# Performance work log

Hardware: AMD Instinct MI355X
Metric: run time of the kernel (lower is better)

Reference implementation:

```python
import jax, jax.numpy as jnp
import numpy as np

K = 16  # neighbors

def _pdist2(a, b):
    # squared euclidean distances (B,N,M); same argsort order as torch.cdist
    return (jnp.sum(a * a, -1)[:, :, None] + jnp.sum(b * b, -1)[:, None, :]
            - 2.0 * jnp.einsum('bnd,bmd->bnm', a, b))

def _knn(xyz, k):
    d2 = jax.lax.stop_gradient(_pdist2(xyz, xyz))
    return jax.lax.top_k(-d2, k)[1]  # (B,N,k) smallest distances

_gather_f = jax.vmap(lambda f, i: f[:, i])  # feat (C,N), idx (...,) -> (C,...)
_gather_x = jax.vmap(lambda x, i: x[i])     # xyz (N,D), idx (...,) -> (...,D)

def _bn_act(x, g, b):
    # eval-mode BatchNorm (running_mean=0, running_var=1) folded to affine, + LeakyReLU(0.1)
    shp = (1, -1) + (1,) * (x.ndim - 2)
    return jax.nn.leaky_relu(x * g.reshape(shp) + b.reshape(shp), 0.1)

def _lfa(xyz, feat, idx, Wm, gm, bm, Ws, Wp, gp, bp):
    # xyz (B,N,3), feat (B,C,N), idx (B,N,K)
    neigh_feat = _gather_f(feat, idx)          # (B,C,N,K)
    neigh_xyz = _gather_x(xyz, idx)            # (B,N,K,3)
    center = xyz[:, :, None, :]
    diff = center - neigh_xyz
    dist = jnp.linalg.norm(diff, axis=-1, keepdims=True)
    rel = jnp.concatenate([diff, dist, jnp.broadcast_to(center, neigh_xyz.shape), neigh_xyz], axis=-1)
    rel = jnp.transpose(rel, (0, 3, 1, 2))     # (B,10,N,K)
    x = jnp.concatenate([neigh_feat, rel], axis=1)          # (B,C+10,N,K)
    x = _bn_act(jnp.einsum('oc,bcnk->bonk', Wm, x), gm, bm)  # (B,O,N,K)
    a = jax.nn.softmax(jnp.einsum('oc,bcnk->bonk', Ws, x), axis=3)
    x = jnp.sum(x * a, axis=3)                               # attentive pool over K -> (B,O,N)
    return _bn_act(jnp.einsum('oc,bcn->bon', Wp, x), gp, bp)

def _interp(src_xyz, src_feat, tgt_xyz):
    nn_idx = jnp.argmin(jax.lax.stop_gradient(_pdist2(tgt_xyz, src_xyz)), axis=-1)  # (B,N)
    return _gather_f(src_feat, nn_idx)  # (B,C,N)


def setup_inputs() -> dict:
    key = jax.random.key(0)
    ks = jax.random.split(key, 24)
    B, N, CIN, NC = 2, 8192, 6, 13
    M1, M2 = N // 2, N // 4
    w = lambda i, shp: jax.random.normal(ks[i], shp, jnp.float32) * 0.05
    ones = lambda c: jnp.ones((c,), jnp.float32)
    zeros = lambda c: jnp.zeros((c,), jnp.float32)
    inp = {
        'xyz': jax.random.uniform(ks[0], (B, N, 3), jnp.float32),
        'feat': jax.random.normal(ks[1], (B, N, CIN), jnp.float32),
        'sel1': jax.random.randint(ks[2], (B, M1), 0, N),
        'sel2': jax.random.randint(ks[3], (B, M2), 0, M1),
        'Wpre': w(4, (64, CIN)), 'gpre': ones(64), 'bpre': zeros(64),
        'W1m': w(5, (64, 74)), 'g1m': ones(64), 'b1m': zeros(64),
        'W1s': w(6, (64, 64)), 'W1p': w(7, (64, 64)), 'g1p': ones(64), 'b1p': zeros(64),
        'W2m': w(8, (128, 74)), 'g2m': ones(128), 'b2m': zeros(128),
        'W2s': w(9, (128, 128)), 'W2p': w(10, (128, 128)), 'g2p': ones(128), 'b2p': zeros(128),
        'W3m': w(11, (256, 138)), 'g3m': ones(256), 'b3m': zeros(256),
        'W3s': w(12, (256, 256)), 'W3p': w(13, (256, 256)), 'g3p': ones(256), 'b3p': zeros(256),
        'Wu2': w(14, (128, 384)), 'gu2': ones(128), 'bu2': zeros(128),
        'Wu1': w(15, (64, 192)), 'gu1': ones(64), 'bu1': zeros(64),
        'Wh1': w(16, (64, 64)), 'bh1': zeros(64),
        'Wh2': w(17, (NC, 64)), 'bh2': zeros(NC),
    }
    return inp


def reference(xyz, feat, sel1, sel2, Wpre, gpre, bpre,
              W1m, g1m, b1m, W1s, W1p, g1p, b1p,
              W2m, g2m, b2m, W2s, W2p, g2p, b2p,
              W3m, g3m, b3m, W3s, W3p, g3p, b3p,
              Wu2, gu2, bu2, Wu1, gu1, bu1,
              Wh1, bh1, Wh2, bh2):
    ft = jnp.transpose(feat, (0, 2, 1))                       # (B,Cin,N)
    x0 = _bn_act(jnp.einsum('oc,bcn->bon', Wpre, ft), gpre, bpre)
    n0 = _knn(xyz, K)
    x1 = _lfa(xyz, x0, n0, W1m, g1m, b1m, W1s, W1p, g1p, b1p)  # (B,64,N)
    xyz1 = _gather_x(xyz, sel1); f1 = _gather_f(x1, sel1)      # random downsample 0.5
    n1 = _knn(xyz1, K)
    x2 = _lfa(xyz1, f1, n1, W2m, g2m, b2m, W2s, W2p, g2p, b2p)  # (B,128,M1)
    xyz2 = _gather_x(xyz1, sel2); f2 = _gather_f(x2, sel2)
    n2 = _knn(xyz2, K)
    x3 = _lfa(xyz2, f2, n2, W3m, g3m, b3m, W3s, W3p, g3p, b3p)  # (B,256,M2)
    up2 = _interp(xyz2, x3, xyz1)
    d2 = _bn_act(jnp.einsum('oc,bcn->bon', Wu2, jnp.concatenate([up2, x2], 1)), gu2, bu2)
    up1 = _interp(xyz1, d2, xyz)
    d1 = _bn_act(jnp.einsum('oc,bcn->bon', Wu1, jnp.concatenate([up1, x1], 1)), gu1, bu1)
    h = jax.nn.leaky_relu(jnp.einsum('oc,bcn->bon', Wh1, d1) + bh1[None, :, None], 0.1)
    logits = jnp.einsum('oc,bcn->bon', Wh2, h) + bh2[None, :, None]
    return jnp.transpose(logits, (0, 2, 1))                    # (B,N,num_classes)
```

## Files before the change

kernel.cpp:

```cpp
#include <hip/hip_runtime.h>
#include <hip/hip_bf16.h>

#pragma clang fp contract(off)

typedef unsigned long long ull;

__device__ __forceinline__ float lrelu(float v) { return v >= 0.0f ? v : 0.1f * v; }

__device__ __forceinline__ float sumsq3(float x, float y, float z) {
    return ((x * x) + (y * y)) + (z * z);
}

__device__ __forceinline__ float dot3fma(float ax, float ay, float az,
                                         float bx, float by, float bz) {
    float d = ax * bx;
    d = __builtin_fmaf(ay, by, d);
    d = __builtin_fmaf(az, bz, d);
    return d;
}

__device__ __forceinline__ float distf(float qn, float sn, float dot) {
    float s = qn + sn;
    return __builtin_fmaf(-2.0f, dot, s);
}

__device__ __forceinline__ ull packkey(float d, int i) {
    unsigned u = __float_as_uint(d);
    u = (u & 0x80000000u) ? ~u : (u | 0x80000000u);
    return ((ull)u << 32) | (unsigned)i;
}

__device__ __forceinline__ ull shfl_xor_u64(ull v, int mask) {
    int lo = __shfl_xor((int)(v & 0xffffffffull), mask);
    int hi = __shfl_xor((int)(v >> 32), mask);
    return ((ull)(unsigned)hi << 32) | (unsigned)lo;
}

__device__ __forceinline__ void cswap64(ull& x, ull& y) {
    bool sw = y < x;
    ull lo = sw ? y : x;
    ull hi = sw ? x : y;
    x = lo; y = hi;
}

__device__ __forceinline__ ull min64(ull a, ull b) { return a < b ? a : b; }

__global__ void k_pre(const float* __restrict__ feat, const float* __restrict__ W,
                      const float* __restrict__ g, const float* __restrict__ bb,
                      float* __restrict__ x0) {
    int p = blockIdx.x * blockDim.x + threadIdx.x;
    if (p >= 2 * 8192) return;
    const float* f = feat + (size_t)p * 6;
    float fv[6];
#pragma unroll
    for (int c = 0; c < 6; ++c) fv[c] = f[c];
    float* out = x0 + (size_t)p * 64;
    for (int o = 0; o < 64; ++o) {
        float s = 0.0f;
#pragma unroll
        for (int c = 0; c < 6; ++c) s = __builtin_fmaf(W[o * 6 + c], fv[c], s);
        float v = s * g[o];
        v = v + bb[o];
        out[o] = lrelu(v);
    }
}

__global__ void k_wt_all(const float* __restrict__ s0, const float* __restrict__ s1,
                         const float* __restrict__ s2, const float* __restrict__ s3,
                         const float* __restrict__ s4, const float* __restrict__ s5,
                         const float* __restrict__ s6, const float* __restrict__ s7,
                         const float* __restrict__ s8,
                         float* __restrict__ d0, float* __restrict__ d1,
                         float* __restrict__ d2, float* __restrict__ d3,
                         float* __restrict__ d4, float* __restrict__ d5,
                         float* __restrict__ d6, float* __restrict__ d7,
                         float* __restrict__ d8) {
    const int Ms[9] = {64, 64, 64, 128, 128, 128, 256, 256, 256};
    const int Ks[9] = {74, 64, 64, 74, 128, 128, 138, 256, 256};
    const float* S[9] = {s0, s1, s2, s3, s4, s5, s6, s7, s8};
    float* D[9] = {d0, d1, d2, d3, d4, d5, d6, d7, d8};
    int seg = blockIdx.y;
    int M = Ms[seg], K = Ks[seg];
    int i = blockIdx.x * 256 + threadIdx.x;
    if (i >= M * K) return;
    int o = i / K, c = i - o * K;
    D[seg][c * M + o] = S[seg][i];
}

template <int LPQ, int TS>
__launch_bounds__(256)
__global__ void k_knn_reg(const float* __restrict__ xyz, int* __restrict__ out_idx, int Npts) {
    constexpr int QPB = 256 / LPQ;
    __shared__ float4 sp[TS];
    int b = blockIdx.y;
    int tid = threadIdx.x;
    int qi = tid / LPQ;
    int l = tid % LPQ;
    int q = blockIdx.x * QPB + qi;
    const float* X = xyz + (size_t)b * Npts * 3;
    float qx = X[q * 3], qy = X[q * 3 + 1], qz = X[q * 3 + 2];
    float qn = sumsq3(qx, qy, qz);

    ull key[16];
#pragma unroll
    for (int u = 0; u < 16; ++u) key[u] = ~0ull;
    ull p0 = ~0ull, p1 = ~0ull, p2 = ~0ull, p3 = ~0ull;
    int cnt = 0;
    float tau_d = INFINITY;

    auto merge = [&]() {
        cswap64(p0, p2); cswap64(p1, p3); cswap64(p0, p1);
        cswap64(p2, p3); cswap64(p1, p2);
        key[12] = min64(key[12], p3);
        key[13] = min64(key[13], p2);
        key[14] = min64(key[14], p1);
        key[15] = min64(key[15], p0);
#pragma unroll
        for (int dstep = 8; dstep >= 1; dstep >>= 1) {
#pragma unroll
            for (int i = 0; i < 16; ++i) {
                if (!(i & dstep)) cswap64(key[i], key[i + dstep]);
            }
        }
        p0 = p1 = p2 = p3 = ~0ull;
        cnt = 0;
        ull t = key[15];
#pragma unroll
        for (int mask = 1; mask < LPQ; mask <<= 1) t = min64(t, shfl_xor_u64(t, mask));
        unsigned hu = (unsigned)(t >> 32);
        unsigned fb = (hu & 0x80000000u) ? (hu & 0x7fffffffu) : ~hu;
        tau_d = (hu == 0xffffffffu) ? INFINITY : __uint_as_float(fb);
    };

    for (int t0 = 0; t0 < Npts; t0 += TS) {
        __syncthreads();
        for (int j = tid; j < TS; j += 256) {
            int i = t0 + j;
            float px = X[i * 3], py = X[i * 3 + 1], pz = X[i * 3 + 2];
            sp[j] = make_float4(px, py, pz, sumsq3(px, py, pz));
        }
        __syncthreads();
        for (int j = l; j < TS; j += LPQ) {
            float4 p = sp[j];
            float d = distf(qn, p.w, dot3fma(qx, qy, qz, p.x, p.y, p.z));
            if (d <= tau_d) {
                p3 = p2; p2 = p1; p1 = p0;
                p0 = packkey(d, t0 + j);
                ++cnt;
            }
            if (__any(cnt >= 4)) merge();
        }
    }
    if (__any(cnt > 0)) merge();

    for (int mask = 1; mask < LPQ; mask <<= 1) {
        ull ok[16];
#pragma unroll
        for (int i = 0; i < 16; ++i) ok[i] = shfl_xor_u64(key[15 - i], mask);
#pragma unroll
        for (int i = 0; i < 16; ++i) key[i] = min64(ok[i], key[i]);
#pragma unroll
        for (int dstep = 8; dstep >= 1; dstep >>= 1) {
#pragma unroll
            for (int i = 0; i < 16; ++i) {
                if (!(i & dstep)) cswap64(key[i], key[i + dstep]);
            }
        }
    }

    if (l == 0) {
        int* o = out_idx + ((size_t)b * Npts + q) * 16;
#pragma unroll
        for (int u = 0; u < 16; ++u) o[u] = (int)(unsigned)(key[u] & 0xffffffffull);
    }
}

template <int C>
__global__ void k_gather(const float* __restrict__ src_xyz, const float* __restrict__ src_feat,
                         const int* __restrict__ sel, float* __restrict__ dst_xyz,
                         float* __restrict__ dst_feat, int M, int Nsrc) {
    int b = blockIdx.y, m = blockIdx.x;
    int s = sel[(size_t)b * M + m];
    const float* fx = src_xyz + ((size_t)b * Nsrc + s) * 3;
    const float* ff = src_feat + ((size_t)b * Nsrc + s) * C;
    float* dx = dst_xyz + ((size_t)b * M + m) * 3;
    float* df = dst_feat + ((size_t)b * M + m) * C;
    if (threadIdx.x < 3) dx[threadIdx.x] = fx[threadIdx.x];
    for (int c = threadIdx.x; c < C; c += blockDim.x) df[c] = ff[c];
}

template <int CIN, int COUT, int NCOL, int THREADS>
__launch_bounds__(THREADS)
__global__ void k_lfa(const float* __restrict__ xyz, const float* __restrict__ feat,
                      const int* __restrict__ kn,
                      const float* __restrict__ WmT, const float* __restrict__ gm, const float* __restrict__ bm,
                      const float* __restrict__ WsT,
                      const float* __restrict__ WpT, const float* __restrict__ gp, const float* __restrict__ bp,
                      float* __restrict__ outf, int Npts) {
    constexpr int CR = CIN + 10;
    constexpr int PPB = NCOL / 16;
    constexpr int BANDS = THREADS / 16;
    constexpr int RT = COUT / BANDS;
    constexpr int CT = NCOL / 16;
    constexpr int TPG = 16 / CT;
    constexpr int BUFR = (CR > COUT) ? CR : COUT;
    static_assert(RT % 4 == 0 && CT % 4 == 0, "geom");
    __shared__ __align__(16) float buf[BUFR * NCOL];
    int b = blockIdx.y, tid = threadIdx.x;
    int n0 = blockIdx.x * PPB;
    const float* X = xyz + (size_t)b * Npts * 3;

    {
        constexpr int TPC = THREADS / NCOL;
        int jl = tid % NCOL;
        int cp = tid / NCOL;
        int n = n0 + (jl >> 4);
        int k = jl & 15;
        int nbr = kn[((size_t)b * Npts + n) * 16 + k];
        const float* fr = feat + ((size_t)b * Npts + nbr) * CIN;
        for (int c = cp; c < CIN; c += TPC) buf[c * NCOL + jl] = fr[c];
        if (cp == 0) {
            float cx = X[n * 3], cy = X[n * 3 + 1], cz = X[n * 3 + 2];
            float nx = X[nbr * 3], ny = X[nbr * 3 + 1], nz = X[nbr * 3 + 2];
            float dx = cx - nx, dy = cy - ny, dz = cz - nz;
            float dn = sqrtf(sumsq3(dx, dy, dz));
            buf[(CIN + 0) * NCOL + jl] = dx; buf[(CIN + 1) * NCOL + jl] = dy;
            buf[(CIN + 2) * NCOL + jl] = dz; buf[(CIN + 3) * NCOL + jl] = dn;
            buf[(CIN + 4) * NCOL + jl] = cx; buf[(CIN + 5) * NCOL + jl] = cy;
            buf[(CIN + 6) * NCOL + jl] = cz; buf[(CIN + 7) * NCOL + jl] = nx;
            buf[(CIN + 8) * NCOL + jl] = ny; buf[(CIN + 9) * NCOL + jl] = nz;
        }
    }
    __syncthreads();

    int tx = tid & 15, ty = tid >> 4;
    float acc[RT][CT];

    auto loadA = [&](float* a, const float* WT, int c) {
#pragma unroll
        for (int r4 = 0; r4 < RT; r4 += 4)
            *reinterpret_cast<float4*>(&a[r4]) =
                *reinterpret_cast<const float4*>(&WT[c * COUT + ty * RT + r4]);
    };
    auto loadB = [&](float* bv, int c) {
#pragma unroll
        for (int c4 = 0; c4 < CT; c4 += 4)
            *reinterpret_cast<float4*>(&bv[c4]) =
                *reinterpret_cast<const float4*>(&buf[c * NCOL + tx * CT + c4]);
    };

#pragma unroll
    for (int r = 0; r < RT; ++r)
#pragma unroll
        for (int cc = 0; cc < CT; ++cc) acc[r][cc] = 0.0f;
    for (int c = 0; c < CR; ++c) {
        float a[RT], bv[CT];
        loadA(a, WmT, c); loadB(bv, c);
#pragma unroll
        for (int r = 0; r < RT; ++r)
#pragma unroll
            for (int cc = 0; cc < CT; ++cc)
                acc[r][cc] = __builtin_fmaf(a[r], bv[cc], acc[r][cc]);
    }
    __syncthreads();
#pragma unroll
    for (int r = 0; r < RT; ++r) {
        int o = ty * RT + r;
        float gg = gm[o], bbv = bm[o];
        float vv[CT];
#pragma unroll
        for (int cc = 0; cc < CT; ++cc) {
            float v = acc[r][cc] * gg;
            v = v + bbv;
            vv[cc] = lrelu(v);
        }
#pragma unroll
        for (int c4 = 0; c4 < CT; c4 += 4)
            *reinterpret_cast<float4*>(&buf[o * NCOL + tx * CT + c4]) =
                *reinterpret_cast<const float4*>(&vv[c4]);
    }
    __syncthreads();

#pragma unroll
    for (int r = 0; r < RT; ++r)
#pragma unroll
        for (int cc = 0; cc < CT; ++cc) acc[r][cc] = 0.0f;
    for (int c = 0; c < COUT; ++c) {
        float a[RT], bv[CT];
        loadA(a, WsT, c); loadB(bv, c);
#pragma unroll
        for (int r = 0; r < RT; ++r)
#pragma unroll
            for (int cc = 0; cc < CT; ++cc)
                acc[r][cc] = __builtin_fmaf(a[r], bv[cc], acc[r][cc]);
    }
    float pwv[RT];
#pragma unroll
    for (int r = 0; r < RT; ++r) {
        int o = ty * RT + r;
        float m = acc[r][0];
#pragma unroll
        for (int cc = 1; cc < CT; ++cc) m = fmaxf(m, acc[r][cc]);
#pragma unroll
        for (int mask = 1; mask < TPG; mask <<= 1) m = fmaxf(m, __shfl_xor(m, mask));
        float e[CT]; float ps = 0.0f;
#pragma unroll
        for (int cc = 0; cc < CT; ++cc) { e[cc] = expf(acc[r][cc] - m); ps = ps + e[cc]; }
        float tot = ps;
#pragma unroll
        for (int mask = 1; mask < TPG; mask <<= 1) tot = tot + __shfl_xor(tot, mask);
        float xm[CT];
#pragma unroll
        for (int c4 = 0; c4 < CT; c4 += 4)
            *reinterpret_cast<float4*>(&xm[c4]) =
                *reinterpret_cast<const float4*>(&buf[o * NCOL + tx * CT + c4]);
        float pw = 0.0f;
#pragma unroll
        for (int cc = 0; cc < CT; ++cc) {
            float a_ = e[cc] / tot;
            float t = xm[cc] * a_;
            pw = pw + t;
        }
#pragma unroll
        for (int mask = 1; mask < TPG; mask <<= 1) pw = pw + __shfl_xor(pw, mask);
        pwv[r] = pw;
    }
    __syncthreads();
    if (tx % TPG == 0) {
        int pt = tx / TPG;
#pragma unroll
        for (int r = 0; r < RT; ++r) buf[(ty * RT + r) * PPB + pt] = pwv[r];
    }
    __syncthreads();

    constexpr int TPP = THREADS / COUT;
    constexpr int NOUT = (PPB + TPP - 1) / TPP;
    int o = tid % COUT;
    int pbase = tid / COUT;
    float sacc[NOUT];
#pragma unroll
    for (int u = 0; u < NOUT; ++u) sacc[u] = 0.0f;
    for (int c = 0; c < COUT; ++c) {
        float wv = WpT[c * COUT + o];
#pragma unroll
        for (int u = 0; u < NOUT; ++u) {
            int p = pbase + u * TPP;
            if (p < PPB) sacc[u] = __builtin_fmaf(wv, buf[c * PPB + p], sacc[u]);
        }
    }
    float gg = gp[o], bbv = bp[o];
#pragma unroll
    for (int u = 0; u < NOUT; ++u) {
        int p = pbase + u * TPP;
        if (p < PPB) {
            float v = sacc[u] * gg;
            v = v + bbv;
            outf[((size_t)b * Npts + n0 + p) * COUT + o] = lrelu(v);
        }
    }
}

template <int LPQ, int TS>
__launch_bounds__(256)
__global__ void k_nn_par(const float* __restrict__ tgt, const float* __restrict__ src,
                         int* __restrict__ nn, int Mt, int Ms) {
    constexpr int QPB = 256 / LPQ;
    __shared__ float4 sp[TS];
    int b = blockIdx.y;
    int tid = threadIdx.x;
    int qi = tid / LPQ;
    int l = tid % LPQ;
    int q = blockIdx.x * QPB + qi;
    const float* T = tgt + (size_t)b * Mt * 3;
    const float* S = src + (size_t)b * Ms * 3;
    float qx = T[q * 3], qy = T[q * 3 + 1], qz = T[q * 3 + 2];
    float qn = sumsq3(qx, qy, qz);
    float bd = INFINITY; int bi = 0x7fffffff;
    for (int t0 = 0; t0 < Ms; t0 += TS) {
        __syncthreads();
        for (int j = tid; j < TS; j += 256) {
            int i = t0 + j;
            float px = S[i * 3], py = S[i * 3 + 1], pz = S[i * 3 + 2];
            sp[j] = make_float4(px, py, pz, sumsq3(px, py, pz));
        }
        __syncthreads();
        for (int j = l; j < TS; j += LPQ) {
            float4 p = sp[j];
            float d = distf(qn, p.w, dot3fma(qx, qy, qz, p.x, p.y, p.z));
            if (d < bd) { bd = d; bi = t0 + j; }
        }
    }
#pragma unroll
    for (int s = LPQ / 2; s; s >>= 1) {
        float od = __shfl_xor(bd, s);
        int oi = __shfl_xor(bi, s);
        bool better = (od < bd) || ((od == bd) && (oi < bi));
        bd = better ? od : bd;
        bi = better ? oi : bi;
    }
    if (l == 0) nn[(size_t)b * Mt + q] = bi;
}

template <int CSRC, int CSKIP, int COUT, int PTS>
__global__ void k_up(const float* __restrict__ srcf, const float* __restrict__ skipf,
                     const int* __restrict__ nn,
                     const float* __restrict__ W, const float* __restrict__ g, const float* __restrict__ bb,
                     float* __restrict__ outf, int Mt, int Ms) {
    constexpr int CTOT = CSRC + CSKIP;
    __shared__ float fin[PTS][CTOT];
    int b = blockIdx.y, tid = threadIdx.x;
    int n0 = blockIdx.x * PTS;
#pragma unroll
    for (int pp = 0; pp < PTS; ++pp) {
        int n = n0 + pp;
        int j = nn[(size_t)b * Mt + n];
        const float* fs = srcf + ((size_t)b * Ms + j) * CSRC;
        const float* fk = skipf + ((size_t)b * Mt + n) * CSKIP;
        for (int c = tid; c < CSRC; c += COUT) fin[pp][c] = fs[c];
        for (int c = tid; c < CSKIP; c += COUT) fin[pp][CSRC + c] = fk[c];
    }
    __syncthreads();
    int o = tid;
    const float* wr = W + (size_t)o * CTOT;
    float s[PTS];
#pragma unroll
    for (int pp = 0; pp < PTS; ++pp) s[pp] = 0.0f;
    for (int c = 0; c < CTOT; ++c) {
        float wv = wr[c];
#pragma unroll
        for (int pp = 0; pp < PTS; ++pp)
            s[pp] = __builtin_fmaf(wv, fin[pp][c], s[pp]);
    }
    float gg = g[o], bbv = bb[o];
#pragma unroll
    for (int pp = 0; pp < PTS; ++pp) {
        float v = s[pp] * gg;
        v = v + bbv;
        outf[((size_t)b * Mt + n0 + pp) * COUT + o] = lrelu(v);
    }
}

__global__ void k_u1head(const float* __restrict__ srcf, const float* __restrict__ skipf,
                         const int* __restrict__ nn,
                         const float* __restrict__ Wu1, const float* __restrict__ gu1, const float* __restrict__ bu1,
                         const float* __restrict__ Wh1, const float* __restrict__ bh1,
                         const float* __restrict__ Wh2, const float* __restrict__ bh2,
                         float* __restrict__ out, int Mt, int Ms) {
    __shared__ float fin[4][192];
    __shared__ float d1[4][64];
    __shared__ float h[4][64];
    int b = blockIdx.y, tid = threadIdx.x;
    int n0 = blockIdx.x * 4;
#pragma unroll
    for (int pp = 0; pp < 4; ++pp) {
        int n = n0 + pp;
        int j = nn[(size_t)b * Mt + n];
        const float* fs = srcf + ((size_t)b * Ms + j) * 128;
        const float* fk = skipf + ((size_t)b * Mt + n) * 64;
        for (int c = tid; c < 128; c += 64) fin[pp][c] = fs[c];
        fin[pp][128 + tid] = fk[tid];
    }
    __syncthreads();
    {
        const float* wr = Wu1 + (size_t)tid * 192;
        float s[4] = {0.0f, 0.0f, 0.0f, 0.0f};
        for (int c = 0; c < 192; ++c) {
            float wv = wr[c];
#pragma unroll
            for (int pp = 0; pp < 4; ++pp)
                s[pp] = __builtin_fmaf(wv, fin[pp][c], s[pp]);
        }
        float gg = gu1[tid], bbv = bu1[tid];
#pragma unroll
        for (int pp = 0; pp < 4; ++pp) {
            float v = s[pp] * gg;
            v = v + bbv;
            d1[pp][tid] = lrelu(v);
        }
    }
    __syncthreads();
    {
        const float* wr = Wh1 + (size_t)tid * 64;
        float s[4] = {0.0f, 0.0f, 0.0f, 0.0f};
        for (int c = 0; c < 64; ++c) {
            float wv = wr[c];
#pragma unroll
            for (int pp = 0; pp < 4; ++pp)
                s[pp] = __builtin_fmaf(wv, d1[pp][c], s[pp]);
        }
        float bbv = bh1[tid];
#pragma unroll
        for (int pp = 0; pp < 4; ++pp) {
            float v = s[pp] + bbv;
            h[pp][tid] = lrelu(v);
        }
    }
    __syncthreads();
    if (tid < 13) {
        const float* wr = Wh2 + (size_t)tid * 64;
        float s[4] = {0.0f, 0.0f, 0.0f, 0.0f};
        for (int c = 0; c < 64; ++c) {
            float wv = wr[c];
#pragma unroll
            for (int pp = 0; pp < 4; ++pp)
                s[pp] = __builtin_fmaf(wv, h[pp][c], s[pp]);
        }
        float bbv = bh2[tid];
#pragma unroll
        for (int pp = 0; pp < 4; ++pp)
            out[((size_t)b * Mt + n0 + pp) * 13 + tid] = s[pp] + bbv;
    }
}

extern "C" void kernel_launch(void* const* d_in, const int* in_sizes, int n_in,
                              void* d_out, int out_size, void* d_ws, size_t ws_size,
                              hipStream_t stream) {
    const float* xyz  = (const float*)d_in[0];
    const float* feat = (const float*)d_in[1];
    const int*   sel1 = (const int*)d_in[2];
    const int*   sel2 = (const int*)d_in[3];
    const float* Wpre = (const float*)d_in[4];
    const float* gpre = (const float*)d_in[5];
    const float* bpre = (const float*)d_in[6];
    const float* W1m  = (const float*)d_in[7];
    const float* g1m  = (const float*)d_in[8];
    const float* b1m  = (const float*)d_in[9];
    const float* W1s  = (const float*)d_in[10];
    const float* W1p  = (const float*)d_in[11];
    const float* g1p  = (const float*)d_in[12];
    const float* b1p  = (const float*)d_in[13];
    const float* W2m  = (const float*)d_in[14];
    const float* g2m  = (const float*)d_in[15];
    const float* b2m  = (const float*)d_in[16];
    const float* W2s  = (const float*)d_in[17];
    const float* W2p  = (const float*)d_in[18];
    const float* g2p  = (const float*)d_in[19];
    const float* b2p  = (const float*)d_in[20];
    const float* W3m  = (const float*)d_in[21];
    const float* g3m  = (const float*)d_in[22];
    const float* b3m  = (const float*)d_in[23];
    const float* W3s  = (const float*)d_in[24];
    const float* W3p  = (const float*)d_in[25];
    const float* g3p  = (const float*)d_in[26];
    const float* b3p  = (const float*)d_in[27];
    const float* Wu2  = (const float*)d_in[28];
    const float* gu2  = (const float*)d_in[29];
    const float* bu2  = (const float*)d_in[30];
    const float* Wu1  = (const float*)d_in[31];
    const float* gu1  = (const float*)d_in[32];
    const float* bu1  = (const float*)d_in[33];
    const float* Wh1  = (const float*)d_in[34];
    const float* bh1  = (const float*)d_in[35];
    const float* Wh2  = (const float*)d_in[36];
    const float* bh2  = (const float*)d_in[37];
    float* out = (float*)d_out;

    char* w = (char*)d_ws;
    auto alloc = [&](size_t n) { char* p = w; w += (n + 255) & ~(size_t)255; return p; };
    float* x0   = (float*)alloc((size_t)2 * 8192 * 64 * 4);
    float* x1   = (float*)alloc((size_t)2 * 8192 * 64 * 4);
    float* f1   = (float*)alloc((size_t)2 * 4096 * 64 * 4);
    float* x2   = (float*)alloc((size_t)2 * 4096 * 128 * 4);
    float* f2   = (float*)alloc((size_t)2 * 2048 * 128 * 4);
    float* x3   = (float*)alloc((size_t)2 * 2048 * 256 * 4);
    float* d2f  = (float*)alloc((size_t)2 * 4096 * 128 * 4);
    float* xyz1 = (float*)alloc((size_t)2 * 4096 * 3 * 4);
    float* xyz2 = (float*)alloc((size_t)2 * 2048 * 3 * 4);
    int* n0   = (int*)alloc((size_t)2 * 8192 * 16 * 4);
    int* n1   = (int*)alloc((size_t)2 * 4096 * 16 * 4);
    int* n2   = (int*)alloc((size_t)2 * 2048 * 16 * 4);
    int* nnu2 = (int*)alloc((size_t)2 * 4096 * 4);
    int* nnu1 = (int*)alloc((size_t)2 * 8192 * 4);
    float* WmT1 = (float*)alloc((size_t)74 * 64 * 4);
    float* WsT1 = (float*)alloc((size_t)64 * 64 * 4);
    float* WpT1 = (float*)alloc((size_t)64 * 64 * 4);
    float* WmT2 = (float*)alloc((size_t)74 * 128 * 4);
    float* WsT2 = (float*)alloc((size_t)128 * 128 * 4);
    float* WpT2 = (float*)alloc((size_t)128 * 128 * 4);
    float* WmT3 = (float*)alloc((size_t)138 * 256 * 4);
    float* WsT3 = (float*)alloc((size_t)256 * 256 * 4);
    float* WpT3 = (float*)alloc((size_t)256 * 256 * 4);

    k_pre<<<128, 128, 0, stream>>>(feat, Wpre, gpre, bpre, x0);
    k_wt_all<<<dim3(256, 9), 256, 0, stream>>>(W1m, W1s, W1p, W2m, W2s, W2p, W3m, W3s, W3p,
                                               WmT1, WsT1, WpT1, WmT2, WsT2, WpT2,
                                               WmT3, WsT3, WpT3);

    k_knn_reg<32, 1024><<<dim3(1024, 2), 256, 0, stream>>>(xyz, n0, 8192);
    k_lfa<64, 64, 128, 256><<<dim3(8192 / 8, 2), 256, 0, stream>>>(
        xyz, x0, n0, WmT1, g1m, b1m, WsT1, WpT1, g1p, b1p, x1, 8192);

    k_gather<64><<<dim3(4096, 2), 64, 0, stream>>>(xyz, x1, sel1, xyz1, f1, 4096, 8192);
    k_knn_reg<32, 1024><<<dim3(512, 2), 256, 0, stream>>>(xyz1, n1, 4096);
    k_lfa<64, 128, 128, 512><<<dim3(4096 / 8, 2), 512, 0, stream>>>(
        xyz1, f1, n1, WmT2, g2m, b2m, WsT2, WpT2, g2p, b2p, x2, 4096);

    k_gather<128><<<dim3(2048, 2), 64, 0, stream>>>(xyz1, x2, sel2, xyz2, f2, 2048, 4096);
    k_knn_reg<32, 1024><<<dim3(256, 2), 256, 0, stream>>>(xyz2, n2, 2048);
    k_lfa<128, 256, 64, 512><<<dim3(2048 / 4, 2), 512, 0, stream>>>(
        xyz2, f2, n2, WmT3, g3m, b3m, WsT3, WpT3, g3p, b3p, x3, 2048);

    k_nn_par<16, 512><<<dim3(256, 2), 256, 0, stream>>>(xyz1, xyz2, nnu2, 4096, 2048);
    k_up<256, 128, 128, 4><<<dim3(1024, 2), 128, 0, stream>>>(x3, x2, nnu2, Wu2, gu2, bu2,
                                                              d2f, 4096, 2048);
    k_nn_par<16, 512><<<dim3(512, 2), 256, 0, stream>>>(xyz, xyz1, nnu1, 8192, 4096);
    k_u1head<<<dim3(2048, 2), 64, 0, stream>>>(d2f, x1, nnu1, Wu1, gu1, bu1, Wh1, bh1,
                                               Wh2, bh2, out, 8192, 4096);
}
```

Before: 1.053 ms.

## Stream LFA weight rows into LDS with async global_load_lds ring pipeline

```diff
diff --git a/kernel.cpp b/kernel.cpp
--- a/kernel.cpp
+++ b/kernel.cpp
@@ -4,6 +4,8 @@
 #pragma clang fp contract(off)
 
 typedef unsigned long long ull;
+typedef const __attribute__((address_space(1))) void GV;
+typedef __attribute__((address_space(3))) void LV;
 
 __device__ __forceinline__ float lrelu(float v) { return v >= 0.0f ? v : 0.1f * v; }
 
@@ -204,8 +206,12 @@
     constexpr int CT = NCOL / 16;
     constexpr int TPG = 16 / CT;
     constexpr int BUFR = (CR > COUT) ? CR : COUT;
+    constexpr int WAVES = THREADS / 64;
+    constexpr int WROWS = 4 * RT;
+    constexpr int DPT = 8;
     static_assert(RT % 4 == 0 && CT % 4 == 0, "geom");
     __shared__ __align__(16) float buf[BUFR * NCOL];
+    __shared__ __align__(16) float wbuf[WAVES * DPT * WROWS];
     int b = blockIdx.y, tid = threadIdx.x;
     int n0 = blockIdx.x * PPB;
     const float* X = xyz + (size_t)b * Npts * 3;
@@ -234,13 +240,25 @@
     __syncthreads();
 
     int tx = tid & 15, ty = tid >> 4;
+    int lane = tid & 63;
+    int wv = tid >> 6;
+    int wrow0 = wv * WROWS;
+    float* mywb = wbuf + wv * (DPT * WROWS);
+
     float acc[RT][CT];
 
-    auto loadA = [&](float* a, const float* WT, int c) {
+    auto stageW = [&](const float* WT, int c, int slot) {
+        if (lane < WROWS) {
+            const float* src = WT + (size_t)c * COUT + wrow0 + lane;
+            __builtin_amdgcn_global_load_lds((GV*)src, (LV*)(mywb + slot * WROWS), 4, 0, 0);
+        }
+    };
+    auto readA = [&](float* a, int slot) {
+        const float* p = mywb + slot * WROWS + (ty & 3) * RT;
 #pragma unroll
         for (int r4 = 0; r4 < RT; r4 += 4)
             *reinterpret_cast<float4*>(&a[r4]) =
-                *reinterpret_cast<const float4*>(&WT[c * COUT + ty * RT + r4]);
+                *reinterpret_cast<const float4*>(&p[r4]);
     };
     auto loadB = [&](float* bv, int c) {
 #pragma unroll
@@ -249,19 +267,44 @@
                 *reinterpret_cast<const float4*>(&buf[c * NCOL + tx * CT + c4]);
     };
 
+    auto run_gemm = [&](const float* __restrict__ WT, int K) {
+#pragma unroll
+        for (int d0 = 0; d0 < DPT; ++d0) stageW(WT, d0, d0);
+        asm volatile("s_waitcnt vmcnt(6)" ::: "memory");
+        __builtin_amdgcn_sched_barrier(0);
+        float aC[RT], bvC[CT], aN[RT], bvN[CT];
+#pragma unroll
+        for (int r = 0; r < RT; ++r) aN[r] = 0.0f;
+#pragma unroll
+        for (int cc = 0; cc < CT; ++cc) bvN[cc] = 0.0f;
+        readA(aC, 0);
+        loadB(bvC, 0);
+        for (int c = 0; c < K; ++c) {
+            if (c + DPT < K) stageW(WT, c + DPT, (c + DPT) & (DPT - 1));
+            if (c + 1 < K) { readA(aN, (c + 1) & (DPT - 1)); loadB(bvN, c + 1); }
+#pragma unroll
+            for (int r = 0; r < RT; ++r)
+#pragma unroll
+                for (int cc = 0; cc < CT; ++cc)
+                    acc[r][cc] = __builtin_fmaf(aC[r], bvC[cc], acc[r][cc]);
+            if (c + DPT < K) {
+                asm volatile("s_waitcnt vmcnt(6)" ::: "memory");
+            } else {
+                asm volatile("s_waitcnt vmcnt(0)" ::: "memory");
+            }
+            __builtin_amdgcn_sched_barrier(0);
+#pragma unroll
+            for (int r = 0; r < RT; ++r) aC[r] = aN[r];
+#pragma unroll
+            for (int cc = 0; cc < CT; ++cc) bvC[cc] = bvN[cc];
+        }
+    };
+
 #pragma unroll
     for (int r = 0; r < RT; ++r)
 #pragma unroll
         for (int cc = 0; cc < CT; ++cc) acc[r][cc] = 0.0f;
-    for (int c = 0; c < CR; ++c) {
-        float a[RT], bv[CT];
-        loadA(a, WmT, c); loadB(bv, c);
-#pragma unroll
-        for (int r = 0; r < RT; ++r)
-#pragma unroll
-            for (int cc = 0; cc < CT; ++cc)
-                acc[r][cc] = __builtin_fmaf(a[r], bv[cc], acc[r][cc]);
-    }
+    run_gemm(WmT, CR);
     __syncthreads();
 #pragma unroll
     for (int r = 0; r < RT; ++r) {
@@ -285,15 +328,7 @@
     for (int r = 0; r < RT; ++r)
 #pragma unroll
         for (int cc = 0; cc < CT; ++cc) acc[r][cc] = 0.0f;
-    for (int c = 0; c < COUT; ++c) {
-        float a[RT], bv[CT];
-        loadA(a, WsT, c); loadB(bv, c);
-#pragma unroll
-        for (int r = 0; r < RT; ++r)
-#pragma unroll
-            for (int cc = 0; cc < CT; ++cc)
-                acc[r][cc] = __builtin_fmaf(a[r], bv[cc], acc[r][cc]);
-    }
+    run_gemm(WsT, COUT);
     float pwv[RT];
 #pragma unroll
     for (int r = 0; r < RT; ++r) {
@@ -341,11 +376,11 @@
 #pragma unroll
     for (int u = 0; u < NOUT; ++u) sacc[u] = 0.0f;
     for (int c = 0; c < COUT; ++c) {
-        float wv = WpT[c * COUT + o];
+        float wv_ = WpT[c * COUT + o];
 #pragma unroll
         for (int u = 0; u < NOUT; ++u) {
             int p = pbase + u * TPP;
-            if (p < PPB) sacc[u] = __builtin_fmaf(wv, buf[c * PPB + p], sacc[u]);
+            if (p < PPB) sacc[u] = __builtin_fmaf(wv_, buf[c * PPB + p], sacc[u]);
         }
     }
     float gg = gp[o], bbv = bp[o];
```

After: 1.271 ms. 1.21x slower.
